# Optimization experiments

Hardware: AMD Instinct MI355X
Metric: run time of the kernel (lower is better)

The kernel has to match this reference:

```python
import jax, jax.numpy as jnp
import numpy as np

N, E, F_IN, H, G, C = 50000, 800000, 128, 128, 64, 10
EPS = 1e-5


def _glorot_lin(key, fin, fout):
    s = 1.0 / np.sqrt(fin)
    return jax.random.uniform(key, (fin, fout), jnp.float32, -s, s)


def setup_inputs() -> dict:
    key = jax.random.key(0)
    ks = jax.random.split(key, 24)
    x = jax.random.normal(ks[0], (N, F_IN), jnp.float32)
    edge_index = jax.random.randint(ks[1], (2, E), 0, N)
    batch = jnp.sort(jax.random.randint(ks[2], (N,), 0, G))
    inp = {"x": x, "edge_index": edge_index, "batch": batch}
    # GCNConv weights [in, out] and biases
    dims = [(F_IN, H), (H, H), (H, H), (H, H)]
    for i, (fi, fo) in enumerate(dims, start=1):
        inp[f"W{i}"] = _glorot_lin(ks[2 + i], fi, fo)
        inp[f"b{i}"] = jnp.zeros((fo,), jnp.float32)
    # BatchNorm affine params
    for i in range(1, 4):
        inp[f"g{i}"] = jnp.ones((H,), jnp.float32)
        inp[f"be{i}"] = jnp.zeros((H,), jnp.float32)
    # MLP head
    inp["lw1"] = _glorot_lin(ks[10], 2 * H, H)
    inp["lb1"] = jnp.zeros((H,), jnp.float32)
    inp["lw2"] = _glorot_lin(ks[11], H, C)
    inp["lb2"] = jnp.zeros((C,), jnp.float32)
    return inp


def _gcn_conv(h_in, W, b, src, dst, norm_e, self_norm):
    # linear transform then symmetric-normalized aggregation (incl. self loops)
    h = h_in @ W                                            # [N, out]
    agg = jax.ops.segment_sum(h[src] * norm_e[:, None], dst, num_segments=N)
    return agg + h * self_norm[:, None] + b


def _batch_norm(x, gamma, beta):
    mu = jnp.mean(x, axis=0)
    var = jnp.var(x, axis=0)
    return (x - mu) * jax.lax.rsqrt(var + EPS) * gamma + beta


def reference(x, edge_index, batch, W1, b1, W2, b2, W3, b3, W4, b4,
              g1, be1, g2, be2, g3, be3, lw1, lb1, lw2, lb2):
    src, dst = edge_index[0], edge_index[1]
    # degrees with self loops; GCN symmetric normalization
    deg = jax.ops.segment_sum(jnp.ones((E,), jnp.float32), dst, num_segments=N) + 1.0
    dinv = jax.lax.rsqrt(deg)
    norm_e = dinv[src] * dinv[dst]   # per-edge norm
    self_norm = 1.0 / deg            # self-loop norm = dinv*dinv

    h = jax.nn.relu(_batch_norm(_gcn_conv(x, W1, b1, src, dst, norm_e, self_norm), g1, be1))
    h = jax.nn.relu(_batch_norm(_gcn_conv(h, W2, b2, src, dst, norm_e, self_norm), g2, be2))
    h = jax.nn.relu(_batch_norm(_gcn_conv(h, W3, b3, src, dst, norm_e, self_norm), g3, be3))
    h = jax.nn.relu(_gcn_conv(h, W4, b4, src, dst, norm_e, self_norm))

    counts = jax.ops.segment_sum(jnp.ones((N,), jnp.float32), batch, num_segments=G)
    x_mean = jax.ops.segment_sum(h, batch, num_segments=G) / counts[:, None]
    x_max = jax.ops.segment_max(h, batch, num_segments=G)
    z = jnp.concatenate([x_mean, x_max], axis=1)            # [G, 2H]

    z = jax.nn.relu(z @ lw1 + lb1)
    # dropout is identity in eval mode
    return z @ lw2 + lb2                                    # [G, C]
```

## Files before the change

kernel.cpp:

```cpp
#include <hip/hip_runtime.h>

#define N_NODES 50000
#define N_EDGES 800000
#define HID     128
#define NGRAPH  64
#define BN_EPS  1e-5f

__global__ __launch_bounds__(256) void deg_counti_kernel(const int* __restrict__ ei,
                                                         int* __restrict__ degi) {
    int i = blockIdx.x * 256 + threadIdx.x;
    if (i < N_EDGES) atomicAdd(&degi[ei[N_EDGES + i]], 1);
}

__global__ __launch_bounds__(256) void deg_fin_kernel(const int* __restrict__ degi,
                                                      float* __restrict__ dinv) {
    int i = blockIdx.x * 256 + threadIdx.x;
    if (i < N_NODES) dinv[i] = rsqrtf((float)degi[i] + 1.0f);
}

__global__ __launch_bounds__(512) void scan_kernel(const int* __restrict__ degi,
                                                   int* __restrict__ row_start) {
    __shared__ int part[512];
    const int t = threadIdx.x;
    const int per = (N_NODES + 511) / 512;
    const int b0 = t * per;
    int s = 0;
    for (int i = b0; i < b0 + per && i < N_NODES; ++i) s += degi[i];
    part[t] = s;
    __syncthreads();
    if (t == 0) {
        int run = 0;
        for (int i = 0; i < 512; ++i) { int v = part[i]; part[i] = run; run += v; }
    }
    __syncthreads();
    int run = part[t];
    for (int i = b0; i < b0 + per && i < N_NODES; ++i) { row_start[i] = run; run += degi[i]; }
    if (t == 511) row_start[N_NODES] = run;
}

__global__ __launch_bounds__(256) void scatter_kernel(const int* __restrict__ ei,
                                                      const float* __restrict__ dinv,
                                                      const int* __restrict__ row_start,
                                                      int* __restrict__ cursor,
                                                      int* __restrict__ csr_src,
                                                      float* __restrict__ csr_w) {
    int e = blockIdx.x * 256 + threadIdx.x;
    if (e >= N_EDGES) return;
    const int src = ei[e];
    const int dst = ei[N_EDGES + e];
    const int pos = row_start[dst] + atomicAdd(&cursor[dst], 1);
    csr_src[pos] = src;
    csr_w[pos] = dinv[src] * dinv[dst];
}

__global__ __launch_bounds__(256) void bounds_kernel(const int* __restrict__ batch,
                                                     int* __restrict__ bound) {
    int i = blockIdx.x * 256 + threadIdx.x;
    if (i >= N_NODES) return;
    const int b = batch[i];
    if (i == 0) {
        for (int g = 0; g <= b; ++g) bound[g] = 0;
    } else {
        const int pb = batch[i - 1];
        for (int g = pb + 1; g <= b; ++g) bound[g] = i;
    }
    if (i == N_NODES - 1) {
        for (int g = b + 1; g <= NGRAPH; ++g) bound[g] = N_NODES;
    }
}

__global__ __launch_bounds__(256) void gemm_kernel(const float* __restrict__ X,
                                                   const float* __restrict__ W,
                                                   const float* __restrict__ bias,
                                                   const float* __restrict__ dinv,
                                                   float* __restrict__ hout,
                                                   float* __restrict__ aggout) {
    __shared__ float xs[64][128];
    const int tid = threadIdx.x;
    const int block_row = blockIdx.x * 64;

    {
        const float4* Xv = (const float4*)(X + (size_t)block_row * HID);
        float4* xsv = (float4*)&xs[0][0];
        int rows_valid = N_NODES - block_row;
        if (rows_valid > 64) rows_valid = 64;
        const int max4 = rows_valid * 32;
        for (int i = tid; i < 64 * 32; i += 256)
            xsv[i] = (i < max4) ? Xv[i] : make_float4(0.f, 0.f, 0.f, 0.f);
    }
    __syncthreads();

    const int cg = (tid & 31) * 4;
    const int r0 = (tid >> 5) * 8;

    float acc[8][4];
#pragma unroll
    for (int r = 0; r < 8; ++r)
#pragma unroll
        for (int j = 0; j < 4; ++j) acc[r][j] = 0.f;

#pragma unroll 4
    for (int k = 0; k < HID; ++k) {
        const float4 w4 = *(const float4*)(W + k * HID + cg);
#pragma unroll
        for (int r = 0; r < 8; ++r) {
            const float xv = xs[r0 + r][k];
            acc[r][0] = fmaf(xv, w4.x, acc[r][0]);
            acc[r][1] = fmaf(xv, w4.y, acc[r][1]);
            acc[r][2] = fmaf(xv, w4.z, acc[r][2]);
            acc[r][3] = fmaf(xv, w4.w, acc[r][3]);
        }
    }

    const float4 bv = *(const float4*)(bias + cg);
#pragma unroll
    for (int r = 0; r < 8; ++r) {
        const int row = block_row + r0 + r;
        if (row < N_NODES) {
            const float dv = dinv[row];
            const float sn = dv * dv;
            float4 hv = make_float4(acc[r][0], acc[r][1], acc[r][2], acc[r][3]);
            *(float4*)(hout + (size_t)row * HID + cg) = hv;
            float4 av = make_float4(fmaf(hv.x, sn, bv.x), fmaf(hv.y, sn, bv.y),
                                    fmaf(hv.z, sn, bv.z), fmaf(hv.w, sn, bv.w));
            *(float4*)(aggout + (size_t)row * HID + cg) = av;
        }
    }
}

__global__ __launch_bounds__(256) void agg_csr_kernel(const int* __restrict__ row_start,
                                                      const int* __restrict__ csr_src,
                                                      const float* __restrict__ csr_w,
                                                      const float* __restrict__ h,
                                                      float* __restrict__ agg) {
    const int node = blockIdx.x * 4 + (threadIdx.x >> 6);
    if (node >= N_NODES) return;
    const int lane = threadIdx.x & 63;
    const int c = lane * 2;
    const int beg = row_start[node];
    const int end = row_start[node + 1];
    float* ap = agg + (size_t)node * HID + c;
    float2 acc = *(const float2*)ap;
    for (int p = beg; p < end; ++p) {
        const int src = csr_src[p];
        const float w = csr_w[p];
        const float2 v = *(const float2*)(h + (size_t)src * HID + c);
        acc.x = fmaf(v.x, w, acc.x);
        acc.y = fmaf(v.y, w, acc.y);
    }
    *(float2*)ap = acc;
}

__global__ __launch_bounds__(256) void bn_stats_kernel(const float* __restrict__ a,
                                                       float* __restrict__ stats) {
    const int c = threadIdx.x & 127;
    const int half = threadIdx.x >> 7;
    const int row0 = blockIdx.x * 128;
    int rend = row0 + 128;
    if (rend > N_NODES) rend = N_NODES;
    float s = 0.f, sq = 0.f;
    for (int r = row0 + half; r < rend; r += 2) {
        const float v = a[(size_t)r * HID + c];
        s += v;
        sq = fmaf(v, v, sq);
    }
    __shared__ float sh[2][2][128];
    sh[0][half][c] = s;
    sh[1][half][c] = sq;
    __syncthreads();
    if (half == 0) {
        atomicAdd(&stats[c], sh[0][0][c] + sh[0][1][c]);
        atomicAdd(&stats[HID + c], sh[1][0][c] + sh[1][1][c]);
    }
}

__global__ __launch_bounds__(128) void bn_fin_kernel(float* __restrict__ stats,
                                                     const float* __restrict__ gamma,
                                                     const float* __restrict__ beta) {
    const int c = threadIdx.x;
    const float invN = 1.0f / (float)N_NODES;
    const float mu = stats[c] * invN;
    const float var = stats[HID + c] * invN - mu * mu;
    const float scale = rsqrtf(var + BN_EPS) * gamma[c];
    stats[c] = scale;
    stats[HID + c] = fmaf(-mu, scale, beta[c]);
}

__global__ __launch_bounds__(256) void bn_apply_kernel(float* __restrict__ a,
                                                       const float* __restrict__ stats) {
    int i = blockIdx.x * 256 + threadIdx.x;
    const int stride = gridDim.x * 256;
    const int total4 = N_NODES * 32;
    for (; i < total4; i += stride) {
        const int c4 = (i & 31) * 4;
        const float4 v = *(const float4*)(a + (size_t)i * 4);
        const float4 sc = *(const float4*)(stats + c4);
        const float4 sh = *(const float4*)(stats + HID + c4);
        float4 o;
        o.x = fmaxf(fmaf(v.x, sc.x, sh.x), 0.f);
        o.y = fmaxf(fmaf(v.y, sc.y, sh.y), 0.f);
        o.z = fmaxf(fmaf(v.z, sc.z, sh.z), 0.f);
        o.w = fmaxf(fmaf(v.w, sc.w, sh.w), 0.f);
        *(float4*)(a + (size_t)i * 4) = o;
    }
}

__global__ __launch_bounds__(256) void pool_seg_kernel(const float* __restrict__ a,
                                                       const int* __restrict__ bound,
                                                       float* __restrict__ z) {
    const int g = blockIdx.x;
    const int cl = threadIdx.x & 31;
    const int c = blockIdx.y * 32 + cl;
    const int par = threadIdx.x >> 5;
    const int beg = bound[g], end = bound[g + 1];
    float s = 0.f, m = 0.f;
    for (int r = beg + par; r < end; r += 8) {
        const float v = fmaxf(a[(size_t)r * HID + c], 0.f);
        s += v;
        m = fmaxf(m, v);
    }
    __shared__ float ssum[8][32];
    __shared__ float smax[8][32];
    ssum[par][cl] = s;
    smax[par][cl] = m;
    __syncthreads();
    if (par == 0) {
        float ts = 0.f, tm = 0.f;
#pragma unroll
        for (int p = 0; p < 8; ++p) { ts += ssum[p][cl]; tm = fmaxf(tm, smax[p][cl]); }
        const float cntf = (float)(end - beg);
        z[g * 256 + c] = ts / fmaxf(cntf, 1.f);
        z[g * 256 + 128 + c] = tm;
    }
}

__global__ __launch_bounds__(128) void head_kernel(const float* __restrict__ z,
                                                   const float* __restrict__ lw1,
                                                   const float* __restrict__ lb1,
                                                   const float* __restrict__ lw2,
                                                   const float* __restrict__ lb2,
                                                   float* __restrict__ out) {
    __shared__ float zin[256];
    __shared__ float z1[128];
    const int g = blockIdx.x;
    const int t = threadIdx.x;
    zin[t] = z[g * 256 + t];
    zin[128 + t] = z[g * 256 + 128 + t];
    __syncthreads();
    float accv = lb1[t];
#pragma unroll 4
    for (int k = 0; k < 256; ++k) accv = fmaf(zin[k], lw1[k * 128 + t], accv);
    z1[t] = fmaxf(accv, 0.f);
    __syncthreads();
    if (t < 10) {
        float o = lb2[t];
#pragma unroll 4
        for (int k = 0; k < 128; ++k) o = fmaf(z1[k], lw2[k * 10 + t], o);
        out[g * 10 + t] = o;
    }
}

extern "C" void kernel_launch(void* const* d_in, const int* in_sizes, int n_in,
                              void* d_out, int out_size, void* d_ws, size_t ws_size,
                              hipStream_t stream) {
    const float* x     = (const float*)d_in[0];
    const int*   ei    = (const int*)d_in[1];
    const int*   batch = (const int*)d_in[2];
    const float* W[4]  = {(const float*)d_in[3], (const float*)d_in[5],
                          (const float*)d_in[7], (const float*)d_in[9]};
    const float* B[4]  = {(const float*)d_in[4], (const float*)d_in[6],
                          (const float*)d_in[8], (const float*)d_in[10]};
    const float* Gm[3] = {(const float*)d_in[11], (const float*)d_in[13],
                          (const float*)d_in[15]};
    const float* Be[3] = {(const float*)d_in[12], (const float*)d_in[14],
                          (const float*)d_in[16]};
    const float* lw1 = (const float*)d_in[17];
    const float* lb1 = (const float*)d_in[18];
    const float* lw2 = (const float*)d_in[19];
    const float* lb2 = (const float*)d_in[20];

    char* ws = (char*)d_ws;
    float* dinv      = (float*)ws;
    float* stats     = (float*)(ws + 50000u * 4);
    float* z         = (float*)(ws + 50256u * 4);
    int*   degi      = (int*)  (ws + 66640u * 4);
    int*   cursor    = (int*)  (ws + 116640u * 4);
    int*   row_start = (int*)  (ws + 166640u * 4);
    int*   bound     = (int*)  (ws + 216644u * 4);
    int*   csr_src   = (int*)  (ws + 216712u * 4);
    float* csr_w     = (float*)(ws + 1016712u * 4);
    float* hbuf      = (float*)(ws + 1816712u * 4);
    float* abuf      = (float*)(ws + 8216712u * 4);

    hipMemsetAsync(degi, 0, 100000u * sizeof(int), stream);
    deg_counti_kernel<<<(N_EDGES + 255) / 256, 256, 0, stream>>>(ei, degi);
    deg_fin_kernel<<<(N_NODES + 255) / 256, 256, 0, stream>>>(degi, dinv);
    scan_kernel<<<1, 512, 0, stream>>>(degi, row_start);
    scatter_kernel<<<(N_EDGES + 255) / 256, 256, 0, stream>>>(ei, dinv, row_start,
                                                              cursor, csr_src, csr_w);
    bounds_kernel<<<(N_NODES + 255) / 256, 256, 0, stream>>>(batch, bound);

    const float* cur = x;
    for (int l = 0; l < 4; ++l) {
        gemm_kernel<<<(N_NODES + 63) / 64, 256, 0, stream>>>(cur, W[l], B[l], dinv,
                                                             hbuf, abuf);
        agg_csr_kernel<<<(N_NODES + 3) / 4, 256, 0, stream>>>(row_start, csr_src,
                                                              csr_w, hbuf, abuf);
        if (l < 3) {
            hipMemsetAsync(stats, 0, 256 * sizeof(float), stream);
            bn_stats_kernel<<<(N_NODES + 127) / 128, 256, 0, stream>>>(abuf, stats);
            bn_fin_kernel<<<1, 128, 0, stream>>>(stats, Gm[l], Be[l]);
            bn_apply_kernel<<<6250, 256, 0, stream>>>(abuf, stats);
        }
        cur = abuf;
    }

    pool_seg_kernel<<<dim3(NGRAPH, 4), 256, 0, stream>>>(abuf, bound, z);
    head_kernel<<<NGRAPH, 128, 0, stream>>>(z, lw1, lb1, lw2, lb2, (float*)d_out);
}
```

Baseline: 920.9 us.

## Fuse BN-apply into GEMM load, self-loop into aggregation, and pack CSR edges

The separate BatchNorm-apply pass is removed. Normalization and ReLU are now applied while the next layer's GEMM loads its input tile into shared memory. The self-loop term and bias move from the GEMM epilogue into the aggregation kernel, so the GEMM writes one output buffer instead of two and aggregation no longer reads a pre-initialized buffer. CSR source index and weight are packed into a single float2, W chunks are staged in shared memory, and the aggregation loop is unrolled by four with independent accumulators for more memory-level parallelism. This cuts several full passes over the 50000x128 activation buffer, at the cost of redoing the BN arithmetic per GEMM tile and some extra shared memory.

```diff
diff --git a/kernel.cpp b/kernel.cpp
--- a/kernel.cpp
+++ b/kernel.cpp
@@ -42,15 +42,16 @@
                                                       const float* __restrict__ dinv,
                                                       const int* __restrict__ row_start,
                                                       int* __restrict__ cursor,
-                                                      int* __restrict__ csr_src,
-                                                      float* __restrict__ csr_w) {
+                                                      float2* __restrict__ csr_sw) {
     int e = blockIdx.x * 256 + threadIdx.x;
     if (e >= N_EDGES) return;
     const int src = ei[e];
     const int dst = ei[N_EDGES + e];
     const int pos = row_start[dst] + atomicAdd(&cursor[dst], 1);
-    csr_src[pos] = src;
-    csr_w[pos] = dinv[src] * dinv[dst];
+    float2 sw;
+    sw.x = __int_as_float(src);
+    sw.y = dinv[src] * dinv[dst];
+    csr_sw[pos] = sw;
 }
 
 __global__ __launch_bounds__(256) void bounds_kernel(const int* __restrict__ batch,
@@ -71,11 +72,11 @@
 
 __global__ __launch_bounds__(256) void gemm_kernel(const float* __restrict__ X,
                                                    const float* __restrict__ W,
-                                                   const float* __restrict__ bias,
-                                                   const float* __restrict__ dinv,
-                                                   float* __restrict__ hout,
-                                                   float* __restrict__ aggout) {
+                                                   const float* __restrict__ stats,
+                                                   const int use_bn,
+                                                   float* __restrict__ hout) {
     __shared__ float xs[64][128];
+    __shared__ float wsm[32][128];
     const int tid = threadIdx.x;
     const int block_row = blockIdx.x * 64;
 
@@ -85,10 +86,20 @@
         int rows_valid = N_NODES - block_row;
         if (rows_valid > 64) rows_valid = 64;
         const int max4 = rows_valid * 32;
-        for (int i = tid; i < 64 * 32; i += 256)
-            xsv[i] = (i < max4) ? Xv[i] : make_float4(0.f, 0.f, 0.f, 0.f);
-    }
-    __syncthreads();
+        for (int i = tid; i < 64 * 32; i += 256) {
+            float4 v = (i < max4) ? Xv[i] : make_float4(0.f, 0.f, 0.f, 0.f);
+            if (use_bn) {
+                const int c4 = (i & 31) * 4;
+                const float4 sc = *(const float4*)(stats + c4);
+                const float4 sh = *(const float4*)(stats + HID + c4);
+                v.x = fmaxf(fmaf(v.x, sc.x, sh.x), 0.f);
+                v.y = fmaxf(fmaf(v.y, sc.y, sh.y), 0.f);
+                v.z = fmaxf(fmaf(v.z, sc.z, sh.z), 0.f);
+                v.w = fmaxf(fmaf(v.w, sc.w, sh.w), 0.f);
+            }
+            xsv[i] = v;
+        }
+    }
 
     const int cg = (tid & 31) * 4;
     const int r0 = (tid >> 5) * 8;
@@ -99,39 +110,43 @@
 #pragma unroll
         for (int j = 0; j < 4; ++j) acc[r][j] = 0.f;
 
-#pragma unroll 4
-    for (int k = 0; k < HID; ++k) {
-        const float4 w4 = *(const float4*)(W + k * HID + cg);
-#pragma unroll
-        for (int r = 0; r < 8; ++r) {
-            const float xv = xs[r0 + r][k];
-            acc[r][0] = fmaf(xv, w4.x, acc[r][0]);
-            acc[r][1] = fmaf(xv, w4.y, acc[r][1]);
-            acc[r][2] = fmaf(xv, w4.z, acc[r][2]);
-            acc[r][3] = fmaf(xv, w4.w, acc[r][3]);
+    for (int kc = 0; kc < 4; ++kc) {
+        __syncthreads();
+        {
+            const float4* Wv = (const float4*)(W + kc * 32 * HID);
+            float4* wsv = (float4*)&wsm[0][0];
+            for (int i = tid; i < 32 * 32; i += 256) wsv[i] = Wv[i];
         }
-    }
-
-    const float4 bv = *(const float4*)(bias + cg);
+        __syncthreads();
+#pragma unroll
+        for (int kk = 0; kk < 32; ++kk) {
+            const float4 w4 = *(const float4*)(&wsm[kk][cg]);
+            const int k = kc * 32 + kk;
+#pragma unroll
+            for (int r = 0; r < 8; ++r) {
+                const float xv = xs[r0 + r][k];
+                acc[r][0] = fmaf(xv, w4.x, acc[r][0]);
+                acc[r][1] = fmaf(xv, w4.y, acc[r][1]);
+                acc[r][2] = fmaf(xv, w4.z, acc[r][2]);
+                acc[r][3] = fmaf(xv, w4.w, acc[r][3]);
+            }
+        }
+    }
+
 #pragma unroll
     for (int r = 0; r < 8; ++r) {
         const int row = block_row + r0 + r;
-        if (row < N_NODES) {
-            const float dv = dinv[row];
-            const float sn = dv * dv;
-            float4 hv = make_float4(acc[r][0], acc[r][1], acc[r][2], acc[r][3]);
-            *(float4*)(hout + (size_t)row * HID + cg) = hv;
-            float4 av = make_float4(fmaf(hv.x, sn, bv.x), fmaf(hv.y, sn, bv.y),
-                                    fmaf(hv.z, sn, bv.z), fmaf(hv.w, sn, bv.w));
-            *(float4*)(aggout + (size_t)row * HID + cg) = av;
-        }
+        if (row < N_NODES)
+            *(float4*)(hout + (size_t)row * HID + cg) =
+                make_float4(acc[r][0], acc[r][1], acc[r][2], acc[r][3]);
     }
 }
 
 __global__ __launch_bounds__(256) void agg_csr_kernel(const int* __restrict__ row_start,
-                                                      const int* __restrict__ csr_src,
-                                                      const float* __restrict__ csr_w,
+                                                      const float2* __restrict__ csr_sw,
                                                       const float* __restrict__ h,
+                                                      const float* __restrict__ dinv,
+                                                      const float* __restrict__ bias,
                                                       float* __restrict__ agg) {
     const int node = blockIdx.x * 4 + (threadIdx.x >> 6);
     if (node >= N_NODES) return;
@@ -139,16 +154,39 @@
     const int c = lane * 2;
     const int beg = row_start[node];
     const int end = row_start[node + 1];
-    float* ap = agg + (size_t)node * HID + c;
-    float2 acc = *(const float2*)ap;
-    for (int p = beg; p < end; ++p) {
-        const int src = csr_src[p];
-        const float w = csr_w[p];
-        const float2 v = *(const float2*)(h + (size_t)src * HID + c);
-        acc.x = fmaf(v.x, w, acc.x);
-        acc.y = fmaf(v.y, w, acc.y);
-    }
-    *(float2*)ap = acc;
+
+    const float dv = dinv[node];
+    const float sn = dv * dv;
+    const float2 hv = *(const float2*)(h + (size_t)node * HID + c);
+    const float2 bv = *(const float2*)(bias + c);
+    float2 a0 = make_float2(fmaf(hv.x, sn, bv.x), fmaf(hv.y, sn, bv.y));
+    float2 a1 = make_float2(0.f, 0.f);
+    float2 a2 = make_float2(0.f, 0.f);
+    float2 a3 = make_float2(0.f, 0.f);
+
+    int p = beg;
+    for (; p + 4 <= end; p += 4) {
+        const float2 e0 = csr_sw[p];
+        const float2 e1 = csr_sw[p + 1];
+        const float2 e2 = csr_sw[p + 2];
+        const float2 e3 = csr_sw[p + 3];
+        const float2 v0 = *(const float2*)(h + (size_t)__float_as_int(e0.x) * HID + c);
+        const float2 v1 = *(const float2*)(h + (size_t)__float_as_int(e1.x) * HID + c);
+        const float2 v2 = *(const float2*)(h + (size_t)__float_as_int(e2.x) * HID + c);
+        const float2 v3 = *(const float2*)(h + (size_t)__float_as_int(e3.x) * HID + c);
+        a0.x = fmaf(v0.x, e0.y, a0.x); a0.y = fmaf(v0.y, e0.y, a0.y);
+        a1.x = fmaf(v1.x, e1.y, a1.x); a1.y = fmaf(v1.y, e1.y, a1.y);
+        a2.x = fmaf(v2.x, e2.y, a2.x); a2.y = fmaf(v2.y, e2.y, a2.y);
+        a3.x = fmaf(v3.x, e3.y, a3.x); a3.y = fmaf(v3.y, e3.y, a3.y);
+    }
+    for (; p < end; ++p) {
+        const float2 e0 = csr_sw[p];
+        const float2 v0 = *(const float2*)(h + (size_t)__float_as_int(e0.x) * HID + c);
+        a0.x = fmaf(v0.x, e0.y, a0.x); a0.y = fmaf(v0.y, e0.y, a0.y);
+    }
+    a0.x += (a1.x + a2.x) + a3.x;
+    a0.y += (a1.y + a2.y) + a3.y;
+    *(float2*)(agg + (size_t)node * HID + c) = a0;
 }
 
 __global__ __launch_bounds__(256) void bn_stats_kernel(const float* __restrict__ a,
@@ -184,25 +222,6 @@
     const float scale = rsqrtf(var + BN_EPS) * gamma[c];
     stats[c] = scale;
     stats[HID + c] = fmaf(-mu, scale, beta[c]);
-}
-
-__global__ __launch_bounds__(256) void bn_apply_kernel(float* __restrict__ a,
-                                                       const float* __restrict__ stats) {
-    int i = blockIdx.x * 256 + threadIdx.x;
-    const int stride = gridDim.x * 256;
-    const int total4 = N_NODES * 32;
-    for (; i < total4; i += stride) {
-        const int c4 = (i & 31) * 4;
-        const float4 v = *(const float4*)(a + (size_t)i * 4);
-        const float4 sc = *(const float4*)(stats + c4);
-        const float4 sh = *(const float4*)(stats + HID + c4);
-        float4 o;
-        o.x = fmaxf(fmaf(v.x, sc.x, sh.x), 0.f);
-        o.y = fmaxf(fmaf(v.y, sc.y, sh.y), 0.f);
-        o.z = fmaxf(fmaf(v.z, sc.z, sh.z), 0.f);
-        o.w = fmaxf(fmaf(v.w, sc.w, sh.w), 0.f);
-        *(float4*)(a + (size_t)i * 4) = o;
-    }
 }
 
 __global__ __launch_bounds__(256) void pool_seg_kernel(const float* __restrict__ a,
@@ -280,37 +299,35 @@
     const float* lb2 = (const float*)d_in[20];
 
     char* ws = (char*)d_ws;
-    float* dinv      = (float*)ws;
-    float* stats     = (float*)(ws + 50000u * 4);
-    float* z         = (float*)(ws + 50256u * 4);
-    int*   degi      = (int*)  (ws + 66640u * 4);
-    int*   cursor    = (int*)  (ws + 116640u * 4);
-    int*   row_start = (int*)  (ws + 166640u * 4);
-    int*   bound     = (int*)  (ws + 216644u * 4);
-    int*   csr_src   = (int*)  (ws + 216712u * 4);
-    float* csr_w     = (float*)(ws + 1016712u * 4);
-    float* hbuf      = (float*)(ws + 1816712u * 4);
-    float* abuf      = (float*)(ws + 8216712u * 4);
+    float*  dinv      = (float*)ws;
+    float*  stats     = (float*)(ws + 50000u * 4);
+    float*  z         = (float*)(ws + 50256u * 4);
+    int*    degi      = (int*)  (ws + 66640u * 4);
+    int*    cursor    = (int*)  (ws + 116640u * 4);
+    int*    row_start = (int*)  (ws + 166640u * 4);
+    int*    bound     = (int*)  (ws + 216644u * 4);
+    float2* csr_sw    = (float2*)(ws + 216712u * 4);
+    float*  hbuf      = (float*)(ws + 1816712u * 4);
+    float*  abuf      = (float*)(ws + 8216712u * 4);
 
     hipMemsetAsync(degi, 0, 100000u * sizeof(int), stream);
     deg_counti_kernel<<<(N_EDGES + 255) / 256, 256, 0, stream>>>(ei, degi);
     deg_fin_kernel<<<(N_NODES + 255) / 256, 256, 0, stream>>>(degi, dinv);
     scan_kernel<<<1, 512, 0, stream>>>(degi, row_start);
     scatter_kernel<<<(N_EDGES + 255) / 256, 256, 0, stream>>>(ei, dinv, row_start,
-                                                              cursor, csr_src, csr_w);
+                                                              cursor, csr_sw);
     bounds_kernel<<<(N_NODES + 255) / 256, 256, 0, stream>>>(batch, bound);
 
     const float* cur = x;
     for (int l = 0; l < 4; ++l) {
-        gemm_kernel<<<(N_NODES + 63) / 64, 256, 0, stream>>>(cur, W[l], B[l], dinv,
-                                                             hbuf, abuf);
-        agg_csr_kernel<<<(N_NODES + 3) / 4, 256, 0, stream>>>(row_start, csr_src,
-                                                              csr_w, hbuf, abuf);
+        gemm_kernel<<<(N_NODES + 63) / 64, 256, 0, stream>>>(cur, W[l], stats,
+                                                             l > 0 ? 1 : 0, hbuf);
+        agg_csr_kernel<<<(N_NODES + 3) / 4, 256, 0, stream>>>(row_start, csr_sw, hbuf,
+                                                              dinv, B[l], abuf);
         if (l < 3) {
             hipMemsetAsync(stats, 0, 256 * sizeof(float), stream);
             bn_stats_kernel<<<(N_NODES + 127) / 128, 256, 0, stream>>>(abuf, stats);
             bn_fin_kernel<<<1, 128, 0, stream>>>(stats, Gm[l], Be[l]);
-            bn_apply_kernel<<<6250, 256, 0, stream>>>(abuf, stats);
         }
         cur = abuf;
     }
```

Result: faster. 827.8 us (-10.1%).
